# Optimization experiments

Hardware: AMD Instinct MI355X
Metric: run time of the kernel (lower is better)

## Reference

```python
import jax, jax.numpy as jnp
import numpy as np
import math

SCALE = math.sqrt(256.0)

def setup_inputs() -> dict:
    key = jax.random.key(0)
    k1, k2, k3, k4, k5 = jax.random.split(key, 5)
    B, C, T, D = 8, 80, 2048, 256
    bound = 1.0 / math.sqrt(C)
    x = jax.random.normal(k1, (B, C, T), dtype=jnp.float32)
    Wk = jax.random.uniform(k2, (D, C), minval=-bound, maxval=bound, dtype=jnp.float32)
    bk = jax.random.uniform(k3, (D,), minval=-bound, maxval=bound, dtype=jnp.float32)
    Wq = jax.random.uniform(k4, (D, C), minval=-bound, maxval=bound, dtype=jnp.float32)
    bq = jax.random.uniform(k5, (D,), minval=-bound, maxval=bound, dtype=jnp.float32)
    return {"x": x, "Wk": Wk, "bk": bk, "Wq": Wq, "bq": bq}

def reference(x, Wk, bk, Wq, bq):
    # x: [B, C=80, T]; work in time-major layout [B, T, C]
    xt = jnp.swapaxes(x, 1, 2)                      # [B, T, C]
    K = xt @ Wk.T + bk                              # [B, T, 256]
    Q = xt @ Wq.T + bq                              # [B, T, 256]
    # softmax over last dim (dim=2 in torch) of K Q^T / sqrt(256)
    att = jax.nn.softmax(jnp.einsum('bid,bjd->bij', K, Q) / SCALE, axis=2)
    # original per-timestep loop is exactly att @ xt (values = raw input, no V proj)
    out = jnp.einsum('bij,bjc->bic', att, xt)       # [B, T, C]
    return jnp.swapaxes(out, 1, 2)                  # [B, C, T]
```

## Files before the change

kernel.cpp:

```cpp
#include <hip/hip_runtime.h>
#include <hip/hip_bf16.h>
#include <math.h>

typedef __bf16 bf16;
typedef __bf16 bf16x8 __attribute__((ext_vector_type(8)));
typedef float  f32x4  __attribute__((ext_vector_type(4)));
typedef float  f32x16 __attribute__((ext_vector_type(16)));
typedef uint32_t u32x4 __attribute__((ext_vector_type(4)));

#define MFMA16(a, b, c) __builtin_amdgcn_mfma_f32_16x16x32_bf16((a), (b), (c), 0, 0, 0)
#define MFMA32(a, b, c) __builtin_amdgcn_mfma_f32_32x32x16_bf16((a), (b), (c), 0, 0, 0)

typedef const uint32_t __attribute__((address_space(1)))* gq_t;
typedef uint32_t __attribute__((address_space(3)))* lq_t;

constexpr int B_ = 8, C_ = 80, T_ = 2048, D_ = 256;
constexpr int NS = 4;
constexpr float LOG2E_16 = 0.090169989f;

static __device__ inline uint32_t pkbf(float lo, float hi) {
  bf16 l = (bf16)lo, h = (bf16)hi;
  uint16_t lb = __builtin_bit_cast(uint16_t, l), hb = __builtin_bit_cast(uint16_t, h);
  return (uint32_t)lb | ((uint32_t)hb << 16);
}

constexpr int VF_TILE = 3 * 2 * 2 * 32 * 8;

__global__ __launch_bounds__(256) void wconv_kernel(
    const float* __restrict__ Wk, const float* __restrict__ bk,
    const float* __restrict__ Wq, const float* __restrict__ bq,
    bf16* __restrict__ Wbf)
{
  const int mat = blockIdx.x, d = threadIdx.x;
  const float* W    = mat ? Wq : Wk;
  const float* bias = mat ? bq : bk;
  bf16* row = Wbf + (size_t)(mat * 256 + d) * 96;
  const float bv = bias[d];
  #pragma unroll
  for (int c8 = 0; c8 < 12; ++c8) {
    bf16x8 o;
    #pragma unroll
    for (int e = 0; e < 8; ++e) {
      int c = c8 * 8 + e;
      float v = (c < 80) ? W[d * C_ + c] : (c == 80 ? bv : 0.f);
      o[e] = (bf16)v;
    }
    *reinterpret_cast<bf16x8*>(row + c8 * 8) = o;
  }
}

__global__ __launch_bounds__(256) void proj_kernel(
    const float* __restrict__ x,
    const bf16* __restrict__ Wbf,
    bf16* __restrict__ Kb,
    bf16* __restrict__ Qb,
    bf16* __restrict__ Vf)
{
  const int t0   = blockIdx.x * 32;
  const int b    = blockIdx.y;
  const int tid  = threadIdx.x;
  const int w    = tid >> 6;
  const int lane = tid & 63;
  const int h    = lane >> 4;
  const int lr   = lane & 15;

  const float* xb = x + (size_t)b * C_ * T_;

  {
    bf16* vout = Vf + (size_t)(b * 64 + blockIdx.x) * VF_TILE;
    #pragma unroll
    for (int g = 0; g < 2; ++g) {
      int f = tid + g * 256;
      if (f < 384) {
        int il2 = f & 31, hi2 = (f >> 5) & 1, kj2 = (f >> 6) & 1, cb2 = f >> 7;
        int c = cb2 * 32 + il2;
        bf16x8 o;
        if (c < 80) {
          const float* sp = xb + (size_t)c * T_ + t0 + kj2 * 16 + hi2 * 8;
          f32x4 v0 = *reinterpret_cast<const f32x4*>(sp);
          f32x4 v1 = *reinterpret_cast<const f32x4*>(sp + 4);
          #pragma unroll
          for (int e = 0; e < 4; ++e) { o[e] = (bf16)v0[e]; o[e + 4] = (bf16)v1[e]; }
        } else {
          #pragma unroll
          for (int e = 0; e < 8; ++e) o[e] = (bf16)0.f;
        }
        *reinterpret_cast<bf16x8*>(vout + f * 8) = o;
      }
    }
  }

  bf16x8 afrag[2][3];
  #pragma unroll
  for (int ib = 0; ib < 2; ++ib) {
    int t = t0 + ib * 16 + lr;
    #pragma unroll
    for (int ks = 0; ks < 3; ++ks) {
      bf16x8 v;
      #pragma unroll
      for (int e = 0; e < 8; ++e) {
        int c = ks * 32 + h * 8 + e;
        float val;
        if (c < 80)       val = xb[c * T_ + t];
        else if (c == 80) val = 1.0f;
        else              val = 0.0f;
        v[e] = (bf16)val;
      }
      afrag[ib][ks] = v;
    }
  }

  const int nb0 = w * 4;
  #pragma unroll
  for (int mat = 0; mat < 2; ++mat) {
    bf16* outp = mat ? Qb : Kb;

    f32x4 acc[2][4];
    #pragma unroll
    for (int ib = 0; ib < 2; ++ib)
      #pragma unroll
      for (int nb = 0; nb < 4; ++nb)
        acc[ib][nb] = f32x4{0.f, 0.f, 0.f, 0.f};

    #pragma unroll
    for (int nb = 0; nb < 4; ++nb) {
      int d = (nb0 + nb) * 16 + lr;
      const bf16* wrow = Wbf + (size_t)(mat * 256 + d) * 96;
      #pragma unroll
      for (int ks = 0; ks < 3; ++ks) {
        bf16x8 bv = *reinterpret_cast<const bf16x8*>(wrow + ks * 32 + h * 8);
        #pragma unroll
        for (int ib = 0; ib < 2; ++ib)
          acc[ib][nb] = MFMA16(afrag[ib][ks], bv, acc[ib][nb]);
      }
    }

    #pragma unroll
    for (int ib = 0; ib < 2; ++ib)
      #pragma unroll
      for (int nb = 0; nb < 4; ++nb) {
        int d = (nb0 + nb) * 16 + lr;
        #pragma unroll
        for (int r = 0; r < 4; ++r) {
          int t = t0 + ib * 16 + h * 4 + r;
          outp[(size_t)(b * T_ + t) * D_ + d] = (bf16)acc[ib][nb][r];
        }
      }
  }
}

__global__ __launch_bounds__(256, 2) void attn_kernel(
    const bf16* __restrict__ Kb,
    const bf16* __restrict__ Qb,
    const bf16* __restrict__ Vf,
    float* __restrict__ Opart,
    float* __restrict__ mpart,
    float* __restrict__ lpart)
{
  constexpr int BN = 32, NT = T_ / BN;
  constexpr int JT_PER = NT / NS;
  __shared__ bf16 qlds[2][BN * D_];

  const int flat = blockIdx.x;
  const int b    = flat & 7;
  const int rem  = flat >> 3;
  const int it   = rem & 15;
  const int s    = rem >> 4;
  const int i0   = it * 128;

  const int tid  = threadIdx.x;
  const int w    = tid >> 6;
  const int lane = tid & 63;
  const int il   = lane & 31;
  const int hi   = lane >> 5;
  const int iw   = i0 + w * 32;

  const bf16* Kbase = Kb + (size_t)b * T_ * D_;
  const bf16* Qbase = Qb + (size_t)b * T_ * D_;
  const bf16* Vbase = Vf + (size_t)b * 64 * VF_TILE;

  bf16x8 kf[16];
  {
    const bf16* kp = Kbase + (size_t)(iw + il) * D_ + hi * 8;
    #pragma unroll
    for (int ks = 0; ks < 16; ++ks)
      kf[ks] = *reinterpret_cast<const bf16x8*>(kp + ks * 16);
  }

  f32x16 oacc[3];
  #pragma unroll
  for (int cb = 0; cb < 3; ++cb)
    #pragma unroll
    for (int r = 0; r < 16; ++r) oacc[cb][r] = 0.f;
  float m_run = -INFINITY, l_run = 0.f;

  const int jt0 = s * JT_PER, jtend = jt0 + JT_PER;
  const int off = (it & 3) * 4;
  auto jmap = [&](int t) { return jt0 + ((t - jt0 + off) & (JT_PER - 1)); };

  auto stage = [&](int jt, int buf) {
    #pragma unroll
    for (int q = 0; q < 4; ++q) {
      int f = tid + 256 * q;
      int j = f >> 5, c = f & 31;
      const bf16* src = Qbase + (size_t)(jt * BN + j) * D_ + ((c ^ j) << 3);
      __builtin_amdgcn_global_load_lds((gq_t)src,
          (lq_t)&qlds[buf][(q * 256 + w * 64) * 8], 16, 0, 0);
    }
  };

  stage(jmap(jt0), 0);
  asm volatile("s_waitcnt vmcnt(0)" ::: "memory");
  __syncthreads();

  int cur = 0;
  for (int t = jt0; t < jtend; ++t, cur ^= 1) {
    const int jt = jmap(t);
    if (t + 1 < jtend) stage(jmap(t + 1), cur ^ 1);

    const bf16* vt = Vbase + (size_t)jt * VF_TILE + lane * 8;
    bf16x8 vf[3][2];
    #pragma unroll
    for (int cb = 0; cb < 3; ++cb)
      #pragma unroll
      for (int kj = 0; kj < 2; ++kj)
        vf[cb][kj] = *reinterpret_cast<const bf16x8*>(vt + (cb * 2 + kj) * 512);

    f32x16 sacc;
    #pragma unroll
    for (int r = 0; r < 16; ++r) sacc[r] = 0.f;
    __builtin_amdgcn_s_setprio(1);
    #pragma unroll
    for (int ks = 0; ks < 16; ++ks) {
      bf16x8 qa = *reinterpret_cast<const bf16x8*>(
          &qlds[cur][il * 256 + (((hi + 2 * ks) ^ il) << 3)]);
      sacc = MFMA32(qa, kf[ks], sacc);
    }
    __builtin_amdgcn_s_setprio(0);

    float p16[16];
    #pragma unroll
    for (int r = 0; r < 16; ++r) p16[r] = sacc[r];
    float mx01 = fmaxf(p16[0], p16[1]),  mx23 = fmaxf(p16[2], p16[3]);
    float mx45 = fmaxf(p16[4], p16[5]),  mx67 = fmaxf(p16[6], p16[7]);
    float mx89 = fmaxf(p16[8], p16[9]),  mxab = fmaxf(p16[10], p16[11]);
    float mxcd = fmaxf(p16[12], p16[13]), mxef = fmaxf(p16[14], p16[15]);
    float mx = fmaxf(fmaxf(fmaxf(mx01, mx23), fmaxf(mx45, mx67)),
                     fmaxf(fmaxf(mx89, mxab), fmaxf(mxcd, mxef)));
    mx = fmaxf(mx, __shfl_xor(mx, 32));

    if (!__all(mx <= m_run + 48.f)) {
      float mnew  = fmaxf(m_run, mx);
      float alpha = exp2f((m_run - mnew) * LOG2E_16);
      m_run = mnew;
      l_run *= alpha;
      #pragma unroll
      for (int cb = 0; cb < 3; ++cb)
        #pragma unroll
        for (int r = 0; r < 16; ++r) oacc[cb][r] *= alpha;
    }
    float rs = 0.f;
    #pragma unroll
    for (int r = 0; r < 16; ++r) {
      p16[r] = exp2f((p16[r] - m_run) * LOG2E_16);
      rs += p16[r];
    }
    l_run += rs;

    uint32_t a0 = pkbf(p16[0],  p16[1]),  a1 = pkbf(p16[2],  p16[3]);
    uint32_t c0 = pkbf(p16[4],  p16[5]),  c1 = pkbf(p16[6],  p16[7]);
    uint32_t a2 = pkbf(p16[8],  p16[9]),  a3 = pkbf(p16[10], p16[11]);
    uint32_t c2 = pkbf(p16[12], p16[13]), c3 = pkbf(p16[14], p16[15]);
    uint32_t a0s = __shfl_xor(a0, 32), a1s = __shfl_xor(a1, 32);
    uint32_t c0s = __shfl_xor(c0, 32), c1s = __shfl_xor(c1, 32);
    uint32_t a2s = __shfl_xor(a2, 32), a3s = __shfl_xor(a3, 32);
    uint32_t c2s = __shfl_xor(c2, 32), c3s = __shfl_xor(c3, 32);
    const bool hh = (hi != 0);
    u32x4 pb0 = { hh ? c0s : a0, hh ? c1s : a1, hh ? c0 : a0s, hh ? c1 : a1s };
    u32x4 pb1 = { hh ? c2s : a2, hh ? c3s : a3, hh ? c2 : a2s, hh ? c3 : a3s };
    bf16x8 pbf0 = __builtin_bit_cast(bf16x8, pb0);
    bf16x8 pbf1 = __builtin_bit_cast(bf16x8, pb1);

    __builtin_amdgcn_s_setprio(1);
    #pragma unroll
    for (int cb = 0; cb < 3; ++cb) {
      oacc[cb] = MFMA32(vf[cb][0], pbf0, oacc[cb]);
      oacc[cb] = MFMA32(vf[cb][1], pbf1, oacc[cb]);
    }
    __builtin_amdgcn_s_setprio(0);

    asm volatile("s_waitcnt vmcnt(0)" ::: "memory");
    __syncthreads();
  }

  l_run += __shfl_xor(l_run, 32);

  float* ob = Opart + (size_t)(s * B_ + b) * C_ * T_;
  #pragma unroll
  for (int cb = 0; cb < 3; ++cb)
    #pragma unroll
    for (int r = 0; r < 16; ++r) {
      if (cb < 2 || r < 8) {
        int c = cb * 32 + (r & 3) + 8 * (r >> 2) + 4 * hi;
        ob[(size_t)c * T_ + iw + il] = oacc[cb][r];
      }
    }
  if (lane < 32) {
    mpart[(size_t)(s * B_ + b) * T_ + iw + il] = m_run;
    lpart[(size_t)(s * B_ + b) * T_ + iw + il] = l_run;
  }
}

__global__ __launch_bounds__(256) void merge_kernel(
    const float* __restrict__ Opart,
    const float* __restrict__ mpart,
    const float* __restrict__ lpart,
    float* __restrict__ out)
{
  const int b      = blockIdx.y;
  const int tid    = threadIdx.x;
  const int slot   = tid & 15;
  const int cstrip = tid >> 4;
  const int t4     = blockIdx.x * 64 + slot * 4;

  f32x4 m[NS], e[NS];
  f32x4 mmax;
  #pragma unroll
  for (int s2 = 0; s2 < NS; ++s2)
    m[s2] = *reinterpret_cast<const f32x4*>(&mpart[(size_t)(s2 * B_ + b) * T_ + t4]);
  #pragma unroll
  for (int r = 0; r < 4; ++r) {
    mmax[r] = m[0][r];
    #pragma unroll
    for (int s2 = 1; s2 < NS; ++s2) mmax[r] = fmaxf(mmax[r], m[s2][r]);
  }
  f32x4 lsum = f32x4{0.f, 0.f, 0.f, 0.f};
  #pragma unroll
  for (int s2 = 0; s2 < NS; ++s2) {
    f32x4 lv = *reinterpret_cast<const f32x4*>(&lpart[(size_t)(s2 * B_ + b) * T_ + t4]);
    #pragma unroll
    for (int r = 0; r < 4; ++r) e[s2][r] = exp2f((m[s2][r] - mmax[r]) * LOG2E_16);
    lsum += e[s2] * lv;
  }
  f32x4 inv;
  #pragma unroll
  for (int r = 0; r < 4; ++r) inv[r] = 1.0f / lsum[r];

  #pragma unroll
  for (int cc = 0; cc < 5; ++cc) {
    const int c = cstrip * 5 + cc;
    f32x4 acc = f32x4{0.f, 0.f, 0.f, 0.f};
    #pragma unroll
    for (int s2 = 0; s2 < NS; ++s2)
      acc += *reinterpret_cast<const f32x4*>(
                 &Opart[((size_t)(s2 * B_ + b) * C_ + c) * T_ + t4]) * e[s2];
    *reinterpret_cast<f32x4*>(&out[((size_t)b * C_ + c) * T_ + t4]) = acc * inv;
  }
}

extern "C" void kernel_launch(void* const* d_in, const int* in_sizes, int n_in,
                              void* d_out, int out_size, void* d_ws, size_t ws_size,
                              hipStream_t stream) {
  (void)in_sizes; (void)n_in; (void)out_size; (void)ws_size;
  const float* x  = (const float*)d_in[0];
  const float* Wk = (const float*)d_in[1];
  const float* bk = (const float*)d_in[2];
  const float* Wq = (const float*)d_in[3];
  const float* bq = (const float*)d_in[4];
  float* out = (float*)d_out;

  char* ws = (char*)d_ws;
  const size_t MB = 1024 * 1024;
  bf16*  Kb    = (bf16*)(ws);
  bf16*  Qb    = (bf16*)(ws + 8 * MB);
  bf16*  Vf    = (bf16*)(ws + 16 * MB);
  bf16*  Wbf   = (bf16*)(ws + 19 * MB);
  float* Opart = (float*)(ws + 20 * MB);
  float* mpart = (float*)(ws + 42 * MB);
  float* lpart = (float*)(ws + 43 * MB);

  dim3 blk(256);
  wconv_kernel<<<dim3(2), blk, 0, stream>>>(Wk, bk, Wq, bq, Wbf);
  dim3 g1(T_ / 32, B_);
  proj_kernel<<<g1, blk, 0, stream>>>(x, Wbf, Kb, Qb, Vf);
  attn_kernel<<<dim3(16 * NS * B_), blk, 0, stream>>>(Kb, Qb, Vf, Opart, mpart, lpart);
  dim3 g3(T_ / 64, B_);
  merge_kernel<<<g3, blk, 0, stream>>>(Opart, mpart, lpart, out);
}
```

Before: 66.62 us.

## Stage 64-row Q tiles per barrier and use permlane32 swap for P repack

The attention loop now stages 64 Q rows per double-buffered LDS stage and processes them as two 32-row halves, so it needs half as many barriers and vmcnt waits. The eight xor-32 shuffles plus selects that repacked the bf16 probabilities are replaced by four permlane32_swap operations. The max and sum reductions are rebalanced into shallower trees. LDS use doubles to 64KB per block, which may reduce occupancy at two blocks per CU.

```diff
diff --git a/kernel.cpp b/kernel.cpp
--- a/kernel.cpp
+++ b/kernel.cpp
@@ -6,6 +6,7 @@
 typedef __bf16 bf16x8 __attribute__((ext_vector_type(8)));
 typedef float  f32x4  __attribute__((ext_vector_type(4)));
 typedef float  f32x16 __attribute__((ext_vector_type(16)));
+typedef uint32_t u32x2 __attribute__((ext_vector_type(2)));
 typedef uint32_t u32x4 __attribute__((ext_vector_type(4)));
 
 #define MFMA16(a, b, c) __builtin_amdgcn_mfma_f32_16x16x32_bf16((a), (b), (c), 0, 0, 0)
@@ -157,8 +158,8 @@
     float* __restrict__ mpart,
     float* __restrict__ lpart)
 {
-  constexpr int BN = 32, NT = T_ / BN;
-  constexpr int JT_PER = NT / NS;
+  constexpr int BN = 64, NSTG = T_ / BN;
+  constexpr int STG_PER = NSTG / NS;
   __shared__ bf16 qlds[2][BN * D_];
 
   const int flat = blockIdx.x;
@@ -194,100 +195,108 @@
     for (int r = 0; r < 16; ++r) oacc[cb][r] = 0.f;
   float m_run = -INFINITY, l_run = 0.f;
 
-  const int jt0 = s * JT_PER, jtend = jt0 + JT_PER;
-  const int off = (it & 3) * 4;
-  auto jmap = [&](int t) { return jt0 + ((t - jt0 + off) & (JT_PER - 1)); };
-
-  auto stage = [&](int jt, int buf) {
-    #pragma unroll
-    for (int q = 0; q < 4; ++q) {
+  const int st0 = s * STG_PER;
+  const int off = (it & 3) * 2;
+  auto smap = [&](int t) { return st0 + ((t - st0 + off) & (STG_PER - 1)); };
+
+  auto stage = [&](int st, int buf) {
+    #pragma unroll
+    for (int q = 0; q < 8; ++q) {
       int f = tid + 256 * q;
       int j = f >> 5, c = f & 31;
-      const bf16* src = Qbase + (size_t)(jt * BN + j) * D_ + ((c ^ j) << 3);
+      const bf16* src = Qbase + (size_t)(st * BN + j) * D_ + ((c ^ (j & 31)) << 3);
       __builtin_amdgcn_global_load_lds((gq_t)src,
           (lq_t)&qlds[buf][(q * 256 + w * 64) * 8], 16, 0, 0);
     }
   };
 
-  stage(jmap(jt0), 0);
+  stage(smap(st0), 0);
   asm volatile("s_waitcnt vmcnt(0)" ::: "memory");
   __syncthreads();
 
   int cur = 0;
-  for (int t = jt0; t < jtend; ++t, cur ^= 1) {
-    const int jt = jmap(t);
-    if (t + 1 < jtend) stage(jmap(t + 1), cur ^ 1);
-
-    const bf16* vt = Vbase + (size_t)jt * VF_TILE + lane * 8;
-    bf16x8 vf[3][2];
-    #pragma unroll
-    for (int cb = 0; cb < 3; ++cb)
-      #pragma unroll
-      for (int kj = 0; kj < 2; ++kj)
-        vf[cb][kj] = *reinterpret_cast<const bf16x8*>(vt + (cb * 2 + kj) * 512);
-
-    f32x16 sacc;
-    #pragma unroll
-    for (int r = 0; r < 16; ++r) sacc[r] = 0.f;
-    __builtin_amdgcn_s_setprio(1);
-    #pragma unroll
-    for (int ks = 0; ks < 16; ++ks) {
-      bf16x8 qa = *reinterpret_cast<const bf16x8*>(
-          &qlds[cur][il * 256 + (((hi + 2 * ks) ^ il) << 3)]);
-      sacc = MFMA32(qa, kf[ks], sacc);
-    }
-    __builtin_amdgcn_s_setprio(0);
-
-    float p16[16];
-    #pragma unroll
-    for (int r = 0; r < 16; ++r) p16[r] = sacc[r];
-    float mx01 = fmaxf(p16[0], p16[1]),  mx23 = fmaxf(p16[2], p16[3]);
-    float mx45 = fmaxf(p16[4], p16[5]),  mx67 = fmaxf(p16[6], p16[7]);
-    float mx89 = fmaxf(p16[8], p16[9]),  mxab = fmaxf(p16[10], p16[11]);
-    float mxcd = fmaxf(p16[12], p16[13]), mxef = fmaxf(p16[14], p16[15]);
-    float mx = fmaxf(fmaxf(fmaxf(mx01, mx23), fmaxf(mx45, mx67)),
-                     fmaxf(fmaxf(mx89, mxab), fmaxf(mxcd, mxef)));
-    mx = fmaxf(mx, __shfl_xor(mx, 32));
-
-    if (!__all(mx <= m_run + 48.f)) {
-      float mnew  = fmaxf(m_run, mx);
-      float alpha = exp2f((m_run - mnew) * LOG2E_16);
-      m_run = mnew;
-      l_run *= alpha;
+  for (int t = st0; t < st0 + STG_PER; ++t, cur ^= 1) {
+    const int st = smap(t);
+    if (t + 1 < st0 + STG_PER) stage(smap(t + 1), cur ^ 1);
+
+    #pragma unroll
+    for (int hf = 0; hf < 2; ++hf) {
+      const int j32 = st * 2 + hf;
+
+      const bf16* vt = Vbase + (size_t)j32 * VF_TILE + lane * 8;
+      bf16x8 vf[3][2];
       #pragma unroll
       for (int cb = 0; cb < 3; ++cb)
         #pragma unroll
-        for (int r = 0; r < 16; ++r) oacc[cb][r] *= alpha;
-    }
-    float rs = 0.f;
-    #pragma unroll
-    for (int r = 0; r < 16; ++r) {
-      p16[r] = exp2f((p16[r] - m_run) * LOG2E_16);
-      rs += p16[r];
-    }
-    l_run += rs;
-
-    uint32_t a0 = pkbf(p16[0],  p16[1]),  a1 = pkbf(p16[2],  p16[3]);
-    uint32_t c0 = pkbf(p16[4],  p16[5]),  c1 = pkbf(p16[6],  p16[7]);
-    uint32_t a2 = pkbf(p16[8],  p16[9]),  a3 = pkbf(p16[10], p16[11]);
-    uint32_t c2 = pkbf(p16[12], p16[13]), c3 = pkbf(p16[14], p16[15]);
-    uint32_t a0s = __shfl_xor(a0, 32), a1s = __shfl_xor(a1, 32);
-    uint32_t c0s = __shfl_xor(c0, 32), c1s = __shfl_xor(c1, 32);
-    uint32_t a2s = __shfl_xor(a2, 32), a3s = __shfl_xor(a3, 32);
-    uint32_t c2s = __shfl_xor(c2, 32), c3s = __shfl_xor(c3, 32);
-    const bool hh = (hi != 0);
-    u32x4 pb0 = { hh ? c0s : a0, hh ? c1s : a1, hh ? c0 : a0s, hh ? c1 : a1s };
-    u32x4 pb1 = { hh ? c2s : a2, hh ? c3s : a3, hh ? c2 : a2s, hh ? c3 : a3s };
-    bf16x8 pbf0 = __builtin_bit_cast(bf16x8, pb0);
-    bf16x8 pbf1 = __builtin_bit_cast(bf16x8, pb1);
-
-    __builtin_amdgcn_s_setprio(1);
-    #pragma unroll
-    for (int cb = 0; cb < 3; ++cb) {
-      oacc[cb] = MFMA32(vf[cb][0], pbf0, oacc[cb]);
-      oacc[cb] = MFMA32(vf[cb][1], pbf1, oacc[cb]);
-    }
-    __builtin_amdgcn_s_setprio(0);
+        for (int kj = 0; kj < 2; ++kj)
+          vf[cb][kj] = *reinterpret_cast<const bf16x8*>(vt + (cb * 2 + kj) * 512);
+
+      f32x16 sacc;
+      #pragma unroll
+      for (int r = 0; r < 16; ++r) sacc[r] = 0.f;
+      __builtin_amdgcn_s_setprio(1);
+      #pragma unroll
+      for (int ks = 0; ks < 16; ++ks) {
+        bf16x8 qa = *reinterpret_cast<const bf16x8*>(
+            &qlds[cur][(hf * 32 + il) * 256 + (((hi + 2 * ks) ^ il) << 3)]);
+        sacc = MFMA32(qa, kf[ks], sacc);
+      }
+      __builtin_amdgcn_s_setprio(0);
+
+      float p16[16];
+      #pragma unroll
+      for (int r = 0; r < 16; ++r) p16[r] = sacc[r];
+      float t0 = fmaxf(fmaxf(p16[0],  p16[1]),  p16[2]);
+      float t1 = fmaxf(fmaxf(p16[3],  p16[4]),  p16[5]);
+      float t2 = fmaxf(fmaxf(p16[6],  p16[7]),  p16[8]);
+      float t3 = fmaxf(fmaxf(p16[9],  p16[10]), p16[11]);
+      float t4 = fmaxf(fmaxf(p16[12], p16[13]), p16[14]);
+      float mx = fmaxf(fmaxf(fmaxf(t0, t1), t2),
+                       fmaxf(fmaxf(t3, t4), p16[15]));
+      mx = fmaxf(mx, __shfl_xor(mx, 32));
+
+      if (!__all(mx <= m_run + 48.f)) {
+        float mnew  = fmaxf(m_run, mx);
+        float alpha = exp2f((m_run - mnew) * LOG2E_16);
+        m_run = mnew;
+        l_run *= alpha;
+        #pragma unroll
+        for (int cb = 0; cb < 3; ++cb)
+          #pragma unroll
+          for (int r = 0; r < 16; ++r) oacc[cb][r] *= alpha;
+      }
+      #pragma unroll
+      for (int r = 0; r < 16; ++r)
+        p16[r] = exp2f((p16[r] - m_run) * LOG2E_16);
+      {
+        float s0 = (p16[0] + p16[1]) + (p16[2] + p16[3]);
+        float s1 = (p16[4] + p16[5]) + (p16[6] + p16[7]);
+        float s2 = (p16[8] + p16[9]) + (p16[10] + p16[11]);
+        float s3 = (p16[12] + p16[13]) + (p16[14] + p16[15]);
+        l_run += (s0 + s1) + (s2 + s3);
+      }
+
+      uint32_t a0 = pkbf(p16[0],  p16[1]),  a1 = pkbf(p16[2],  p16[3]);
+      uint32_t c0 = pkbf(p16[4],  p16[5]),  c1 = pkbf(p16[6],  p16[7]);
+      uint32_t a2 = pkbf(p16[8],  p16[9]),  a3 = pkbf(p16[10], p16[11]);
+      uint32_t c2 = pkbf(p16[12], p16[13]), c3 = pkbf(p16[14], p16[15]);
+      u32x2 w0 = __builtin_amdgcn_permlane32_swap(a0, c0, false, false);
+      u32x2 w1 = __builtin_amdgcn_permlane32_swap(a1, c1, false, false);
+      u32x2 w2 = __builtin_amdgcn_permlane32_swap(a2, c2, false, false);
+      u32x2 w3 = __builtin_amdgcn_permlane32_swap(a3, c3, false, false);
+      u32x4 pb0 = { w0[0], w1[0], w0[1], w1[1] };
+      u32x4 pb1 = { w2[0], w3[0], w2[1], w3[1] };
+      bf16x8 pbf0 = __builtin_bit_cast(bf16x8, pb0);
+      bf16x8 pbf1 = __builtin_bit_cast(bf16x8, pb1);
+
+      __builtin_amdgcn_s_setprio(1);
+      #pragma unroll
+      for (int cb = 0; cb < 3; ++cb) {
+        oacc[cb] = MFMA32(vf[cb][0], pbf0, oacc[cb]);
+        oacc[cb] = MFMA32(vf[cb][1], pbf1, oacc[cb]);
+      }
+      __builtin_amdgcn_s_setprio(0);
+    }
 
     asm volatile("s_waitcnt vmcnt(0)" ::: "memory");
     __syncthreads();
```

Result: faster. 64.59 us (-3.0%).
